# Performance work log

Measured on AMD Instinct MI355X. Metric: run time of the kernel, lower is better.

## Reference

```python
import jax, jax.numpy as jnp
import numpy as np

B, N, QDIM = 2, 4096, 768
H, D = 8, 64  # num_head, head_dim; inner_dim = 512
INNER = H * D


def setup_inputs() -> dict:
    key = jax.random.key(0)
    ks = jax.random.split(key, 6)
    s = lambda fan_in: 1.0 / np.sqrt(fan_in)
    return {
        "x": jax.random.normal(ks[0], (B, N, QDIM), dtype=jnp.float32),
        "Wq": jax.random.normal(ks[1], (QDIM, INNER), dtype=jnp.float32) * s(QDIM),
        "Wk": jax.random.normal(ks[2], (QDIM, INNER), dtype=jnp.float32) * s(QDIM),
        "Wv": jax.random.normal(ks[3], (QDIM, INNER), dtype=jnp.float32) * s(QDIM),
        "Wout": jax.random.normal(ks[4], (INNER, QDIM), dtype=jnp.float32) * s(INNER),
        "b_out": jnp.zeros((QDIM,), dtype=jnp.float32),
    }


def reference(x, Wq, Wk, Wv, Wout, b_out):
    # x: [b, n, q_dim]; self-attention (kv = x), no mask, dropout = 0 (eval).
    scale = D ** -0.5
    # project and split heads: [b, n, h*d] -> [b, h, n, d]
    def heads(t):
        b, n, _ = t.shape
        return t.reshape(b, n, H, D).transpose(0, 2, 1, 3)
    q = heads(x @ Wq)
    k = heads(x @ Wk)
    v = heads(x @ Wv)
    qk = jnp.einsum("bhid,bhjd->bhij", q, k) * scale  # [b, h, n, n] -- O(n^2) matrix
    attn = jax.nn.softmax(qk, axis=-1)
    out = jnp.einsum("bhij,bhjd->bhid", attn, v)  # [b, h, n, d]
    out = out.transpose(0, 2, 1, 3).reshape(x.shape[0], x.shape[1], INNER)
    return out @ Wout + b_out
```

## Files before the change

kernel.cpp:

```cpp
#include <hip/hip_runtime.h>
#include <cstdint>
#include <cstddef>


typedef __attribute__((ext_vector_type(8))) short short8;
typedef __attribute__((ext_vector_type(4))) float f32x4;
typedef __attribute__((ext_vector_type(16))) float f32x16;
typedef __attribute__((ext_vector_type(4))) unsigned int uint4v;

__device__ __forceinline__ unsigned short f2bf(float f) {
  unsigned int u = __float_as_uint(f);
  u = (u + 0x7fffu + ((u >> 16) & 1u)) >> 16;
  return (unsigned short)u;
}

__device__ __forceinline__ float fast_exp2(float x) {
#if __has_builtin(__builtin_amdgcn_exp2f)
  return __builtin_amdgcn_exp2f(x);
#else
  return __expf(x * 0.69314718055994531f);
#endif
}

__device__ __forceinline__ void gld16(const void* g, void* l) {
  __builtin_amdgcn_global_load_lds(
      (__attribute__((address_space(1))) void*)const_cast<void*>(g),
      (__attribute__((address_space(3))) void*)l, 16, 0, 0);
}

__device__ __forceinline__ unsigned int cvtpk_bf16(float lo, float hi) {
  unsigned int r;
  asm("v_cvt_pk_bf16_f32 %0, %1, %2" : "=v"(r) : "v"(lo), "v"(hi));
  return r;
}


__global__ __launch_bounds__(256) void cvt_x_k(const float* __restrict__ x,
                                               unsigned short* __restrict__ xb) {
  const size_t i = ((size_t)blockIdx.x * 256 + threadIdx.x) * 4;
  const float4 v = *(const float4*)(x + i);
  ushort4 u;
  u.x = f2bf(v.x); u.y = f2bf(v.y); u.z = f2bf(v.z); u.w = f2bf(v.w);
  *(ushort4*)(xb + i) = u;
}

__global__ __launch_bounds__(256) void transpose_w_k(
    const float* __restrict__ Wq, const float* __restrict__ Wk,
    const float* __restrict__ Wv, const float* __restrict__ Wout,
    unsigned short* __restrict__ Wt,
    unsigned short* __restrict__ WoT)
{
  __shared__ float t[32][33];
  const int z = blockIdx.z;
  const float* src = (z == 0) ? Wq : (z == 1) ? Wk : (z == 2) ? Wv : Wout;
  const int R = (z < 3) ? 768 : 512, C = (z < 3) ? 512 : 768;
  unsigned short* dst = (z < 3) ? (Wt + (size_t)z * 393216) : WoT;
  const int tx = threadIdx.x & 31, ty = threadIdx.x >> 5;
  const int c0 = blockIdx.x * 32, r0 = blockIdx.y * 32;
  if (c0 >= C || r0 >= R) return;
#pragma unroll
  for (int k = 0; k < 4; ++k)
    t[ty + 8 * k][tx] = src[(size_t)(r0 + ty + 8 * k) * C + c0 + tx];
  __syncthreads();
#pragma unroll
  for (int k = 0; k < 4; ++k)
    dst[(size_t)(c0 + ty + 8 * k) * R + r0 + tx] = f2bf(t[tx][ty + 8 * k]);
}


__global__ __launch_bounds__(256) void gemm_qkv_k(
    const unsigned short* __restrict__ A,
    const unsigned short* __restrict__ Wt,
    unsigned short* __restrict__ qb, unsigned short* __restrict__ kb,
    unsigned short* __restrict__ vtb) {
  __shared__ __align__(16) short Al[4096];
  __shared__ __align__(16) short Bl[4096];
  const int tid = threadIdx.x;
  const int w = tid >> 6, lane = tid & 63, quad = lane >> 4, l15 = lane & 15;
  const int wy = w >> 1, wx = w & 1;
  const int m0 = blockIdx.x * 128, n0 = blockIdx.y * 128;
  const int z = blockIdx.z;
  const unsigned short* Bt = Wt + (size_t)z * (512 * 768);

  f32x4 acc[4][4];
#pragma unroll
  for (int i = 0; i < 4; ++i)
#pragma unroll
    for (int j = 0; j < 4; ++j) acc[i][j] = (f32x4){0.f, 0.f, 0.f, 0.f};

  for (int k0 = 0; k0 < 768; k0 += 32) {
    __syncthreads();
#pragma unroll
    for (int s = 0; s < 2; ++s) {
      const int t = s * 256 + tid;
      gld16(A + (size_t)(m0 + (t >> 2)) * 768 + k0 + (t & 3) * 8,
            Al + s * 2048 + w * 512);
      gld16(Bt + (size_t)(n0 + (t >> 2)) * 768 + k0 + (t & 3) * 8,
            Bl + s * 2048 + w * 512);
    }
    __syncthreads();
    short8 af[4], bf[4];
#pragma unroll
    for (int i = 0; i < 4; ++i) {
      af[i] = *(const short8*)(Al + (wy * 64 + i * 16 + l15) * 32 + quad * 8);
      bf[i] = *(const short8*)(Bl + (wx * 64 + i * 16 + l15) * 32 + quad * 8);
    }
    if (z == 2) {
#pragma unroll
      for (int i = 0; i < 4; ++i)
#pragma unroll
        for (int j = 0; j < 4; ++j)
          acc[i][j] = __builtin_amdgcn_mfma_f32_16x16x32_bf16(af[i], bf[j], acc[i][j], 0, 0, 0);
    } else {
#pragma unroll
      for (int i = 0; i < 4; ++i)
#pragma unroll
        for (int j = 0; j < 4; ++j)
          acc[i][j] = __builtin_amdgcn_mfma_f32_16x16x32_bf16(bf[i], af[j], acc[i][j], 0, 0, 0);
    }
  }

  if (z == 2) {
#pragma unroll
    for (int i = 0; i < 4; ++i) {
#pragma unroll
      for (int j = 0; j < 4; ++j) {
        const int m0r = m0 + wy * 64 + i * 16 + quad * 4;
        const int n = n0 + wx * 64 + j * 16 + l15;
        const int b = m0r >> 12, nseq0 = m0r & 4095;
        const int h = n >> 6, d0 = n & 63;
        const int kti = nseq0 >> 5, kc = (nseq0 >> 4) & 1;
        const int hv = (nseq0 >> 3) & 1, e0 = nseq0 & 7;
        const int dt = (d0 >> 5) & 1, lv = hv * 32 + (d0 & 31);
        ushort4 u;
        u.x = f2bf(acc[i][j][0]); u.y = f2bf(acc[i][j][1]);
        u.z = f2bf(acc[i][j][2]); u.w = f2bf(acc[i][j][3]);
        *(ushort4*)(vtb + (size_t)(b * 8 + h) * 262144 +
                    ((((kti * 2 + dt) * 2 + kc) * 64 + lv) * 8 + e0)) = u;
      }
    }
  } else {
    const float qs = 0.18033688011112042f;
#pragma unroll
    for (int i = 0; i < 4; ++i) {
#pragma unroll
      for (int j = 0; j < 4; ++j) {
        const int n0r = n0 + wx * 64 + i * 16 + quad * 4;
        const int m = m0 + wy * 64 + j * 16 + l15;
        const int b = m >> 12, nseq = m & 4095;
        const int h = n0r >> 6, d0 = n0r & 63;
        ushort4 u;
        if (z == 0) {
          u.x = f2bf(acc[i][j][0] * qs); u.y = f2bf(acc[i][j][1] * qs);
          u.z = f2bf(acc[i][j][2] * qs); u.w = f2bf(acc[i][j][3] * qs);
          *(ushort4*)(qb + (size_t)((b * 8 + h) * 4096 + nseq) * 64 + d0) = u;
        } else {
          const int kti = nseq >> 5, l31k = nseq & 31;
          const int c = (d0 >> 4) & 3, hk = (d0 >> 3) & 1, e0 = d0 & 7;
          u.x = f2bf(acc[i][j][0]); u.y = f2bf(acc[i][j][1]);
          u.z = f2bf(acc[i][j][2]); u.w = f2bf(acc[i][j][3]);
          *(ushort4*)(kb + (size_t)(b * 8 + h) * 262144 +
                      (((kti * 4 + c) * 64 + (hk * 32 + l31k)) * 8 + e0)) = u;
        }
      }
    }
  }
}


__global__ __launch_bounds__(256) void attn_k(
    const unsigned short* __restrict__ qb,
    const unsigned short* __restrict__ kb,
    const unsigned short* __restrict__ vtb,
    unsigned short* __restrict__ ob) {
  __shared__ __align__(16) char smem[34816];
  const int tid = threadIdx.x;
  const int w = tid >> 6, lane = tid & 63;
  const int l31 = lane & 31, hi = lane >> 5;
  const int g = w >> 1, wq = w & 1;

  const int L = blockIdx.x + 32 * blockIdx.y;
  const int bh = ((L & 7) << 1) | ((L >> 3) & 1);
  const int q0 = (L >> 4) << 7;

  const unsigned short* qbase = qb + (size_t)bh * (4096 * 64);
  const unsigned short* kbase = kb + (size_t)bh * 262144 + lane * 8;
  const unsigned short* vbase = vtb + (size_t)bh * 262144 + lane * 8;

  short8 qf[2][4];
#pragma unroll
  for (int qs = 0; qs < 2; ++qs) {
    const int qrow = q0 + wq * 64 + qs * 32 + l31;
#pragma unroll
    for (int c = 0; c < 4; ++c)
      qf[qs][c] = *(const short8*)(qbase + (size_t)qrow * 64 + c * 16 + hi * 8);
  }

  f32x16 Oacc[2][2];
#pragma unroll
  for (int qs = 0; qs < 2; ++qs)
#pragma unroll
    for (int dt = 0; dt < 2; ++dt)
#pragma unroll
      for (int r = 0; r < 16; ++r) Oacc[qs][dt][r] = 0.f;
  float lsum[2] = {0.f, 0.f};

  const int jbase = g * 2048;

#define LOADKV(KF, VF, JJ, KT)                                                   \
  {                                                                              \
    const int kti_ = ((JJ) >> 5) + (KT);                                         \
    _Pragma("unroll")                                                            \
    for (int c = 0; c < 4; ++c)                                                  \
      KF[c] = *(const short8*)(kbase + (size_t)(kti_ * 4 + c) * 512);            \
    _Pragma("unroll")                                                            \
    for (int dt = 0; dt < 2; ++dt)                                               \
      _Pragma("unroll")                                                          \
      for (int kc = 0; kc < 2; ++kc)                                             \
        VF[dt][kc] = *(const short8*)(vbase +                                    \
                                      (size_t)((kti_ * 2 + dt) * 2 + kc) * 512); \
  }

  auto compute = [&](const short8 (&kf)[4], const short8 (&vfr)[2][2]) {
    uint4v pa[2][2];
#pragma unroll
    for (int qs = 0; qs < 2; ++qs) {
      f32x16 s;
#pragma unroll
      for (int r = 0; r < 16; ++r) s[r] = 0.f;
#pragma unroll
      for (int c = 0; c < 4; ++c)
        s = __builtin_amdgcn_mfma_f32_32x32x16_bf16(kf[c], qf[qs][c], s, 0, 0, 0);

      float e[16];
#pragma unroll
      for (int r = 0; r < 16; ++r) e[r] = fast_exp2(s[r]);
      lsum[qs] += (((e[0] + e[1]) + (e[2] + e[3])) + ((e[4] + e[5]) + (e[6] + e[7]))) +
                  (((e[8] + e[9]) + (e[10] + e[11])) + ((e[12] + e[13]) + (e[14] + e[15])));

      unsigned int wv[8];
#pragma unroll
      for (int g2 = 0; g2 < 4; ++g2)
#pragma unroll
        for (int p = 0; p < 2; ++p)
          wv[g2 * 2 + p] = cvtpk_bf16(e[4 * g2 + 2 * p], e[4 * g2 + 2 * p + 1]);

      const unsigned int s0 = hi ? wv[0] : wv[2];
      const unsigned int s1 = hi ? wv[1] : wv[3];
      const unsigned int s2 = hi ? wv[4] : wv[6];
      const unsigned int s3 = hi ? wv[5] : wv[7];
      const unsigned int x0 = __shfl_xor(s0, 32, 64);
      const unsigned int x1 = __shfl_xor(s1, 32, 64);
      const unsigned int x2 = __shfl_xor(s2, 32, 64);
      const unsigned int x3 = __shfl_xor(s3, 32, 64);
      pa[qs][0] = (uint4v){hi ? x0 : wv[0], hi ? x1 : wv[1],
                           hi ? wv[2] : x0, hi ? wv[3] : x1};
      pa[qs][1] = (uint4v){hi ? x2 : wv[4], hi ? x3 : wv[5],
                           hi ? wv[6] : x2, hi ? wv[7] : x3};
    }

#pragma unroll
    for (int dt = 0; dt < 2; ++dt)
#pragma unroll
      for (int kc = 0; kc < 2; ++kc)
#pragma unroll
        for (int qs = 0; qs < 2; ++qs)
          Oacc[qs][dt] = __builtin_amdgcn_mfma_f32_32x32x16_bf16(
              __builtin_bit_cast(short8, pa[qs][kc]), vfr[dt][kc], Oacc[qs][dt], 0, 0, 0);
  };

  short8 kfA[4], kfB[4];
  short8 vfA[2][2], vfB[2][2];
  LOADKV(kfA, vfA, jbase, 0);

  for (int j0 = 0; j0 < 2048; j0 += 64) {
    const int jj = jbase + j0;
    LOADKV(kfB, vfB, jj, 1);
    compute(kfA, vfA);
    const int jn = (j0 + 64 < 2048) ? (jj + 64) : jbase;
    LOADKV(kfA, vfA, jn, 0);
    compute(kfB, vfB);
  }
#undef LOADKV

  float lt[2];
#pragma unroll
  for (int qs = 0; qs < 2; ++qs)
    lt[qs] = lsum[qs] + __shfl_xor(lsum[qs], 32, 64);

  __syncthreads();
  float* Ox = (float*)smem;
  float* Lx = (float*)(smem + 33792);
#pragma unroll
  for (int qs = 0; qs < 2; ++qs)
    Lx[g * 128 + wq * 64 + qs * 32 + l31] = lt[qs];
  if (g == 1) {
#pragma unroll
    for (int qs = 0; qs < 2; ++qs)
#pragma unroll
      for (int dt = 0; dt < 2; ++dt)
#pragma unroll
        for (int r = 0; r < 16; ++r) {
          const int row = wq * 64 + qs * 32 + (r & 3) + 8 * (r >> 2) + 4 * hi;
          Ox[row * 66 + dt * 32 + l31] = Oacc[qs][dt][r];
        }
  }
  __syncthreads();
  if (g == 0) {
    const int b = bh >> 3, h = bh & 7;
#pragma unroll
    for (int qs = 0; qs < 2; ++qs)
#pragma unroll
      for (int r = 0; r < 16; ++r) {
        const int row = wq * 64 + qs * 32 + (r & 3) + 8 * (r >> 2) + 4 * hi;
        const float inv = 1.0f / (Lx[row] + Lx[128 + row]);
#pragma unroll
        for (int dt = 0; dt < 2; ++dt)
          ob[(size_t)(b * 4096 + q0 + row) * 512 + h * 64 + dt * 32 + l31] =
              f2bf((Oacc[qs][dt][r] + Ox[row * 66 + dt * 32 + l31]) * inv);
      }
  }
}


__global__ __launch_bounds__(256) void gemm_out_k(
    const unsigned short* __restrict__ A,
    const unsigned short* __restrict__ Bt,
    const float* __restrict__ bias, float* __restrict__ out) {
  __shared__ __align__(16) short Al[4096];
  __shared__ __align__(16) short Bl[2048];
  const int tid = threadIdx.x;
  const int w = tid >> 6, lane = tid & 63, quad = lane >> 4, l15 = lane & 15;
  const int m0 = blockIdx.x * 128, n0 = blockIdx.y * 64;

  f32x4 acc[2][4];
#pragma unroll
  for (int i = 0; i < 2; ++i)
#pragma unroll
    for (int j = 0; j < 4; ++j) acc[i][j] = (f32x4){0.f, 0.f, 0.f, 0.f};

  for (int k0 = 0; k0 < 512; k0 += 32) {
    __syncthreads();
#pragma unroll
    for (int s = 0; s < 2; ++s) {
      const int t = s * 256 + tid;
      gld16(A + (size_t)(m0 + (t >> 2)) * 512 + k0 + (t & 3) * 8,
            Al + s * 2048 + w * 512);
    }
    gld16(Bt + (size_t)(n0 + (tid >> 2)) * 512 + k0 + (tid & 3) * 8,
          Bl + w * 512);
    __syncthreads();
    short8 af[2], bf[4];
#pragma unroll
    for (int i = 0; i < 2; ++i)
      af[i] = *(const short8*)(Al + (w * 32 + i * 16 + l15) * 32 + quad * 8);
#pragma unroll
    for (int j = 0; j < 4; ++j)
      bf[j] = *(const short8*)(Bl + (j * 16 + l15) * 32 + quad * 8);
#pragma unroll
    for (int i = 0; i < 2; ++i)
#pragma unroll
      for (int j = 0; j < 4; ++j)
        acc[i][j] = __builtin_amdgcn_mfma_f32_16x16x32_bf16(bf[j], af[i], acc[i][j], 0, 0, 0);
  }

#pragma unroll
  for (int i = 0; i < 2; ++i) {
#pragma unroll
    for (int j = 0; j < 4; ++j) {
      const int col0 = n0 + j * 16 + quad * 4;
      const int m = m0 + w * 32 + i * 16 + l15;
      const float4 b4 = *(const float4*)(bias + col0);
      float4 o;
      o.x = acc[i][j][0] + b4.x; o.y = acc[i][j][1] + b4.y;
      o.z = acc[i][j][2] + b4.z; o.w = acc[i][j][3] + b4.w;
      *(float4*)(out + (size_t)m * 768 + col0) = o;
    }
  }
}


extern "C" void kernel_launch(void* const* d_in, const int* in_sizes, int n_in,
                              void* d_out, int out_size, void* d_ws, size_t ws_size,
                              hipStream_t stream) {
  const float* x    = (const float*)d_in[0];
  const float* Wq   = (const float*)d_in[1];
  const float* Wk   = (const float*)d_in[2];
  const float* Wv   = (const float*)d_in[3];
  const float* Wout = (const float*)d_in[4];
  const float* bout = (const float*)d_in[5];
  float* out = (float*)d_out;
  char* ws = (char*)d_ws;

  unsigned short* xb  = (unsigned short*)(ws);
  unsigned short* Wt  = (unsigned short*)(ws + 12582912);
  unsigned short* WoT = (unsigned short*)(ws + 14942208);
  unsigned short* qb  = (unsigned short*)(ws + 15728640);
  unsigned short* kb  = (unsigned short*)(ws + 24117248);
  unsigned short* vtb = (unsigned short*)(ws + 32505856);
  unsigned short* ob  = (unsigned short*)(ws + 40894464);

  cvt_x_k<<<6144, 256, 0, stream>>>(x, xb);
  transpose_w_k<<<dim3(24, 24, 4), 256, 0, stream>>>(Wq, Wk, Wv, Wout, Wt, WoT);
  gemm_qkv_k<<<dim3(64, 4, 3), 256, 0, stream>>>(xb, Wt, qb, kb, vtb);
  attn_k<<<dim3(32, 16), 256, 0, stream>>>(qb, kb, vtb, ob);
  gemm_out_k<<<dim3(64, 12), 256, 0, stream>>>(ob, WoT, bout, out);
}
```

Before: 219.9 us.

## Halve attention query tile per block, drop K/V double-buffering for occupancy

The attention kernel now processes 64 query rows per block instead of 128, giving each wave one 32-row Q slice, and launches twice as many blocks. The manual register double-buffering of K/V fragments is removed in favour of loading inside the loop, and launch bounds request 4 blocks per SM. The aim is to cut register and LDS pressure so more waves are resident and latency is hidden by occupancy. In exchange, each K/V fragment loaded from global memory is reused across half as many query rows, which doubles K/V traffic per query.

```diff
diff --git a/kernel.cpp b/kernel.cpp
--- a/kernel.cpp
+++ b/kernel.cpp
@@ -168,75 +168,70 @@
 }
 
 
-__global__ __launch_bounds__(256) void attn_k(
+__global__ __launch_bounds__(256, 4) void attn_k(
     const unsigned short* __restrict__ qb,
     const unsigned short* __restrict__ kb,
     const unsigned short* __restrict__ vtb,
     unsigned short* __restrict__ ob) {
-  __shared__ __align__(16) char smem[34816];
+  __shared__ __align__(16) char smem[17408];
   const int tid = threadIdx.x;
   const int w = tid >> 6, lane = tid & 63;
   const int l31 = lane & 31, hi = lane >> 5;
   const int g = w >> 1, wq = w & 1;
 
-  const int L = blockIdx.x + 32 * blockIdx.y;
+  const int L = blockIdx.x + 64 * blockIdx.y;
   const int bh = ((L & 7) << 1) | ((L >> 3) & 1);
-  const int q0 = (L >> 4) << 7;
+  const int q0 = (L >> 4) << 6;
 
   const unsigned short* qbase = qb + (size_t)bh * (4096 * 64);
   const unsigned short* kbase = kb + (size_t)bh * 262144 + lane * 8;
   const unsigned short* vbase = vtb + (size_t)bh * 262144 + lane * 8;
 
-  short8 qf[2][4];
-#pragma unroll
-  for (int qs = 0; qs < 2; ++qs) {
-    const int qrow = q0 + wq * 64 + qs * 32 + l31;
+  short8 qf[4];
+  {
+    const int qrow = q0 + wq * 32 + l31;
 #pragma unroll
     for (int c = 0; c < 4; ++c)
-      qf[qs][c] = *(const short8*)(qbase + (size_t)qrow * 64 + c * 16 + hi * 8);
-  }
-
-  f32x16 Oacc[2][2];
-#pragma unroll
-  for (int qs = 0; qs < 2; ++qs)
-#pragma unroll
-    for (int dt = 0; dt < 2; ++dt)
-#pragma unroll
-      for (int r = 0; r < 16; ++r) Oacc[qs][dt][r] = 0.f;
-  float lsum[2] = {0.f, 0.f};
+      qf[c] = *(const short8*)(qbase + (size_t)qrow * 64 + c * 16 + hi * 8);
+  }
+
+  f32x16 Oacc[2];
+#pragma unroll
+  for (int dt = 0; dt < 2; ++dt)
+#pragma unroll
+    for (int r = 0; r < 16; ++r) Oacc[dt][r] = 0.f;
+  float lsum = 0.f;
 
   const int jbase = g * 2048;
 
-#define LOADKV(KF, VF, JJ, KT)                                                   \
-  {                                                                              \
-    const int kti_ = ((JJ) >> 5) + (KT);                                         \
-    _Pragma("unroll")                                                            \
-    for (int c = 0; c < 4; ++c)                                                  \
-      KF[c] = *(const short8*)(kbase + (size_t)(kti_ * 4 + c) * 512);            \
-    _Pragma("unroll")                                                            \
-    for (int dt = 0; dt < 2; ++dt)                                               \
-      _Pragma("unroll")                                                          \
-      for (int kc = 0; kc < 2; ++kc)                                             \
-        VF[dt][kc] = *(const short8*)(vbase +                                    \
-                                      (size_t)((kti_ * 2 + dt) * 2 + kc) * 512); \
-  }
-
-  auto compute = [&](const short8 (&kf)[4], const short8 (&vfr)[2][2]) {
-    uint4v pa[2][2];
-#pragma unroll
-    for (int qs = 0; qs < 2; ++qs) {
+  for (int j0 = 0; j0 < 2048; j0 += 64) {
+    const int kti0 = (jbase + j0) >> 5;
+#pragma unroll
+    for (int kt = 0; kt < 2; ++kt) {
+      const int kti = kti0 + kt;
+      short8 kf[4];
+#pragma unroll
+      for (int c = 0; c < 4; ++c)
+        kf[c] = *(const short8*)(kbase + (size_t)(kti * 4 + c) * 512);
+      short8 vf[2][2];
+#pragma unroll
+      for (int dt = 0; dt < 2; ++dt)
+#pragma unroll
+        for (int kc = 0; kc < 2; ++kc)
+          vf[dt][kc] = *(const short8*)(vbase + (size_t)((kti * 2 + dt) * 2 + kc) * 512);
+
       f32x16 s;
 #pragma unroll
       for (int r = 0; r < 16; ++r) s[r] = 0.f;
 #pragma unroll
       for (int c = 0; c < 4; ++c)
-        s = __builtin_amdgcn_mfma_f32_32x32x16_bf16(kf[c], qf[qs][c], s, 0, 0, 0);
+        s = __builtin_amdgcn_mfma_f32_32x32x16_bf16(kf[c], qf[c], s, 0, 0, 0);
 
       float e[16];
 #pragma unroll
       for (int r = 0; r < 16; ++r) e[r] = fast_exp2(s[r]);
-      lsum[qs] += (((e[0] + e[1]) + (e[2] + e[3])) + ((e[4] + e[5]) + (e[6] + e[7]))) +
-                  (((e[8] + e[9]) + (e[10] + e[11])) + ((e[12] + e[13]) + (e[14] + e[15])));
+      lsum += (((e[0] + e[1]) + (e[2] + e[3])) + ((e[4] + e[5]) + (e[6] + e[7]))) +
+              (((e[8] + e[9]) + (e[10] + e[11])) + ((e[12] + e[13]) + (e[14] + e[15])));
 
       unsigned int wv[8];
 #pragma unroll
@@ -253,72 +248,48 @@
       const unsigned int x1 = __shfl_xor(s1, 32, 64);
       const unsigned int x2 = __shfl_xor(s2, 32, 64);
       const unsigned int x3 = __shfl_xor(s3, 32, 64);
-      pa[qs][0] = (uint4v){hi ? x0 : wv[0], hi ? x1 : wv[1],
-                           hi ? wv[2] : x0, hi ? wv[3] : x1};
-      pa[qs][1] = (uint4v){hi ? x2 : wv[4], hi ? x3 : wv[5],
-                           hi ? wv[6] : x2, hi ? wv[7] : x3};
-    }
-
-#pragma unroll
-    for (int dt = 0; dt < 2; ++dt)
-#pragma unroll
-      for (int kc = 0; kc < 2; ++kc)
-#pragma unroll
-        for (int qs = 0; qs < 2; ++qs)
-          Oacc[qs][dt] = __builtin_amdgcn_mfma_f32_32x32x16_bf16(
-              __builtin_bit_cast(short8, pa[qs][kc]), vfr[dt][kc], Oacc[qs][dt], 0, 0, 0);
-  };
-
-  short8 kfA[4], kfB[4];
-  short8 vfA[2][2], vfB[2][2];
-  LOADKV(kfA, vfA, jbase, 0);
-
-  for (int j0 = 0; j0 < 2048; j0 += 64) {
-    const int jj = jbase + j0;
-    LOADKV(kfB, vfB, jj, 1);
-    compute(kfA, vfA);
-    const int jn = (j0 + 64 < 2048) ? (jj + 64) : jbase;
-    LOADKV(kfA, vfA, jn, 0);
-    compute(kfB, vfB);
-  }
-#undef LOADKV
-
-  float lt[2];
-#pragma unroll
-  for (int qs = 0; qs < 2; ++qs)
-    lt[qs] = lsum[qs] + __shfl_xor(lsum[qs], 32, 64);
+      uint4v pa[2];
+      pa[0] = (uint4v){hi ? x0 : wv[0], hi ? x1 : wv[1],
+                       hi ? wv[2] : x0, hi ? wv[3] : x1};
+      pa[1] = (uint4v){hi ? x2 : wv[4], hi ? x3 : wv[5],
+                       hi ? wv[6] : x2, hi ? wv[7] : x3};
+
+#pragma unroll
+      for (int dt = 0; dt < 2; ++dt)
+#pragma unroll
+        for (int kc = 0; kc < 2; ++kc)
+          Oacc[dt] = __builtin_amdgcn_mfma_f32_32x32x16_bf16(
+              __builtin_bit_cast(short8, pa[kc]), vf[dt][kc], Oacc[dt], 0, 0, 0);
+    }
+  }
+
+  const float lt = lsum + __shfl_xor(lsum, 32, 64);
 
   __syncthreads();
   float* Ox = (float*)smem;
-  float* Lx = (float*)(smem + 33792);
-#pragma unroll
-  for (int qs = 0; qs < 2; ++qs)
-    Lx[g * 128 + wq * 64 + qs * 32 + l31] = lt[qs];
+  float* Lx = (float*)(smem + 16896);
+  Lx[g * 64 + wq * 32 + l31] = lt;
   if (g == 1) {
 #pragma unroll
-    for (int qs = 0; qs < 2; ++qs)
-#pragma unroll
-      for (int dt = 0; dt < 2; ++dt)
-#pragma unroll
-        for (int r = 0; r < 16; ++r) {
-          const int row = wq * 64 + qs * 32 + (r & 3) + 8 * (r >> 2) + 4 * hi;
-          Ox[row * 66 + dt * 32 + l31] = Oacc[qs][dt][r];
-        }
+    for (int dt = 0; dt < 2; ++dt)
+#pragma unroll
+      for (int r = 0; r < 16; ++r) {
+        const int row = wq * 32 + (r & 3) + 8 * (r >> 2) + 4 * hi;
+        Ox[row * 66 + dt * 32 + l31] = Oacc[dt][r];
+      }
   }
   __syncthreads();
   if (g == 0) {
     const int b = bh >> 3, h = bh & 7;
 #pragma unroll
-    for (int qs = 0; qs < 2; ++qs)
-#pragma unroll
-      for (int r = 0; r < 16; ++r) {
-        const int row = wq * 64 + qs * 32 + (r & 3) + 8 * (r >> 2) + 4 * hi;
-        const float inv = 1.0f / (Lx[row] + Lx[128 + row]);
-#pragma unroll
-        for (int dt = 0; dt < 2; ++dt)
-          ob[(size_t)(b * 4096 + q0 + row) * 512 + h * 64 + dt * 32 + l31] =
-              f2bf((Oacc[qs][dt][r] + Ox[row * 66 + dt * 32 + l31]) * inv);
-      }
+    for (int r = 0; r < 16; ++r) {
+      const int row = wq * 32 + (r & 3) + 8 * (r >> 2) + 4 * hi;
+      const float inv = 1.0f / (Lx[row] + Lx[64 + row]);
+#pragma unroll
+      for (int dt = 0; dt < 2; ++dt)
+        ob[(size_t)(b * 4096 + q0 + row) * 512 + h * 64 + dt * 32 + l31] =
+            f2bf((Oacc[dt][r] + Ox[row * 66 + dt * 32 + l31]) * inv);
+    }
   }
 }
 
@@ -403,6 +374,6 @@
   cvt_x_k<<<6144, 256, 0, stream>>>(x, xb);
   transpose_w_k<<<dim3(24, 24, 4), 256, 0, stream>>>(Wq, Wk, Wv, Wout, Wt, WoT);
   gemm_qkv_k<<<dim3(64, 4, 3), 256, 0, stream>>>(xb, Wt, qb, kb, vtb);
-  attn_k<<<dim3(32, 16), 256, 0, stream>>>(qb, kb, vtb, ob);
+  attn_k<<<dim3(64, 16), 256, 0, stream>>>(qb, kb, vtb, ob);
   gemm_out_k<<<dim3(64, 12), 256, 0, stream>>>(ob, WoT, bout, out);
 }
```

Result: slower. 252.7 us (+14.9%).
